# Optimization experiments

Hardware: AMD Instinct MI355X
Metric: run time of the kernel (lower is better)

Reference implementation:

```python
import jax, jax.numpy as jnp
import numpy as np

EMBED_DIM = 1024
NUM_HEADS = 16
HEAD_DIM = EMBED_DIM // NUM_HEADS
SCALE = float(np.sqrt(HEAD_DIM))
B, TQ, TK = 2, 2048, 2048


def setup_inputs() -> dict:
    key = jax.random.key(0)
    ks = jax.random.split(key, 16)
    s = 1.0 / np.sqrt(EMBED_DIM)
    inp = {
        "query": jax.random.normal(ks[0], (B, TQ, EMBED_DIM), jnp.float32),
        "key": jax.random.normal(ks[1], (B, TK, EMBED_DIM), jnp.float32),
        "value": jax.random.normal(ks[2], (B, TK, EMBED_DIM), jnp.float32),
        "key_padding_mask": jnp.zeros((B, TK), dtype=bool),
        "Wq": jax.random.uniform(ks[3], (EMBED_DIM, EMBED_DIM), jnp.float32, -s, s),
        "bq": jax.random.uniform(ks[4], (EMBED_DIM,), jnp.float32, -s, s),
        "Wk": jax.random.uniform(ks[5], (EMBED_DIM, EMBED_DIM), jnp.float32, -s, s),
        "bk": jax.random.uniform(ks[6], (EMBED_DIM,), jnp.float32, -s, s),
        "Wv": jax.random.uniform(ks[7], (EMBED_DIM, EMBED_DIM), jnp.float32, -s, s),
        "bv": jax.random.uniform(ks[8], (EMBED_DIM,), jnp.float32, -s, s),
        "Wo": jax.random.uniform(ks[9], (EMBED_DIM, EMBED_DIM), jnp.float32, -s, s),
        "bo": jax.random.uniform(ks[10], (EMBED_DIM,), jnp.float32, -s, s),
        "clr_bias_q": jax.random.normal(ks[11], (NUM_HEADS, 1, HEAD_DIM), jnp.float32) * 0.02,
        "clr_bias_k": jax.random.normal(ks[12], (NUM_HEADS, 1, HEAD_DIM), jnp.float32) * 0.02,
    }
    return inp


def reference(query, key, value, key_padding_mask, Wq, bq, Wk, bk, Wv, bv, Wo, bo,
              clr_bias_q, clr_bias_k):
    Bsz, Tq, _ = query.shape
    Tk = key.shape[1]

    def split_heads(x, W, b, T):
        # Linear (torch convention: x @ W.T + b) then [B, H, T, Dh]
        y = jnp.einsum('bte,fe->btf', x, W) + b
        return y.reshape(Bsz, T, NUM_HEADS, HEAD_DIM).transpose(0, 2, 1, 3)

    q = split_heads(query, Wq, bq, Tq)   # [B,H,Tq,Dh]
    k = split_heads(key, Wk, bk, Tk)     # [B,H,Tk,Dh]
    v = split_heads(value, Wv, bv, Tk)   # [B,H,Tk,Dh]

    # CLR centering + learned bias (Aitchison similarity)
    q_c = q - jnp.mean(q, axis=-1, keepdims=True) + clr_bias_q[None]
    k_c = k - jnp.mean(k, axis=-1, keepdims=True) + clr_bias_k[None]
    scores = jnp.einsum('bhqd,bhkd->bhqk', q_c, k_c) / SCALE  # [B,H,Tq,Tk]

    mask = key_padding_mask[:, None, None, :]  # [B,1,1,Tk], True = ignore
    scores = jnp.where(mask, -jnp.inf, scores)

    attn = jax.nn.softmax(scores, axis=-1)
    out = jnp.einsum('bhqk,bhkd->bhqd', attn, v)
    out = out.transpose(0, 2, 1, 3).reshape(Bsz, Tq, EMBED_DIM)
    return jnp.einsum('bte,fe->btf', out, Wo) + bo
```

## Files before the change

### kernel.cpp

```cpp
#include <hip/hip_runtime.h>
#include <stdint.h>

static constexpr int EMB   = 1024;
static constexpr int HEADS = 16;
static constexpr int HD    = 64;
static constexpr int BATCH = 2;
static constexpr int SEQ   = 2048;
static constexpr int BT    = BATCH * SEQ;
static constexpr float QSC = 0.18033688011112042f;

typedef short   short8  __attribute__((ext_vector_type(8)));
typedef float   float4v __attribute__((ext_vector_type(4)));

__device__ __forceinline__ ushort f2bf(float f) {
    union { float f; uint32_t i; } v; v.f = f;
    uint32_t x = v.i;
    return (ushort)((x + 0x7FFFu + ((x >> 16) & 1u)) >> 16);
}
__device__ __forceinline__ uint32_t pack2bf(float lo, float hi) {
    union { float f; uint32_t u; } a, b; a.f = lo; b.f = hi;
    uint32_t ra = a.u + 0x7FFFu + ((a.u >> 16) & 1u);
    uint32_t rb = b.u + 0x7FFFu + ((b.u >> 16) & 1u);
    return (rb & 0xFFFF0000u) | (ra >> 16);
}
__device__ __forceinline__ float fast_exp2(float x) {
#if __has_builtin(__builtin_amdgcn_exp2f)
    return __builtin_amdgcn_exp2f(x);
#else
    return exp2f(x);
#endif
}

__device__ __forceinline__ void async_ld16(const void* g, void* l) {
    __builtin_amdgcn_global_load_lds(
        (const __attribute__((address_space(1))) void*)g,
        (__attribute__((address_space(3))) void*)l,
        16, 0, 0);
}

__global__ void cvt_all(const float* __restrict__ q, const float* __restrict__ k,
                        const float* __restrict__ v,
                        const float* __restrict__ wq, const float* __restrict__ wk,
                        const float* __restrict__ wv, const float* __restrict__ wo,
                        ushort* __restrict__ qb, ushort* __restrict__ kb,
                        ushort* __restrict__ vb,
                        ushort* __restrict__ wqb, ushort* __restrict__ wkb,
                        ushort* __restrict__ wvb, ushort* __restrict__ wob)
{
    int bid = blockIdx.x;
    const float* src; ushort* dst; size_t off;
    if (bid < 6144) {
        int seg = bid >> 11;
        src = seg == 0 ? q : (seg == 1 ? k : v);
        dst = seg == 0 ? qb : (seg == 1 ? kb : vb);
        off = (size_t)(bid & 2047) * 2048;
    } else {
        int t = bid - 6144, seg = t >> 9;
        src = seg == 0 ? wq : (seg == 1 ? wk : (seg == 2 ? wv : wo));
        dst = seg == 0 ? wqb : (seg == 1 ? wkb : (seg == 2 ? wvb : wob));
        off = (size_t)(t & 511) * 2048;
    }
    size_t base = off + (size_t)threadIdx.x * 8;
    float4 a0 = *(const float4*)(src + base);
    float4 a1 = *(const float4*)(src + base + 4);
    uint32_t o[4] = { pack2bf(a0.x, a0.y), pack2bf(a0.z, a0.w),
                      pack2bf(a1.x, a1.y), pack2bf(a1.z, a1.w) };
    *(uint4*)(dst + base) = *(uint4*)o;
}

__device__ __forceinline__ void gemm_core_128(
    const ushort* __restrict__ A, const ushort* __restrict__ W,
    int m0, int n0, int K,
    ushort* As, ushort* Ws,
    int wid, int lane, float4v acc[4][4])
{
    const int lrow8 = lane >> 3;
    const int gc    = (lane & 7) ^ lrow8;
    const ushort* Ab = A + (size_t)m0 * K + gc * 8;
    const ushort* Wb = W + (size_t)n0 * K + gc * 8;
    const int wm = (wid >> 1) * 64;
    const int wn = (wid & 1) * 64;

    for (int k0 = 0; k0 < K; k0 += 64) {
        __syncthreads();
#pragma unroll
        for (int it = 0; it < 4; ++it) {
            int rg = it * 4 + wid;
            int row = rg * 8 + lrow8;
            async_ld16(Ab + (size_t)row * K + k0, &As[rg * 512]);
            async_ld16(Wb + (size_t)row * K + k0, &Ws[rg * 512]);
        }
        __syncthreads();
#pragma unroll
        for (int ks = 0; ks < 2; ++ks) {
            const int c = ks * 4 + (lane >> 4);
            short8 af[4], wf[4];
#pragma unroll
            for (int i = 0; i < 4; i++) {
                int row = wm + i * 16 + (lane & 15);
                af[i] = *(const short8*)&As[row * 64 + ((c ^ (row & 7)) * 8)];
            }
#pragma unroll
            for (int j = 0; j < 4; j++) {
                int row = wn + j * 16 + (lane & 15);
                wf[j] = *(const short8*)&Ws[row * 64 + ((c ^ (row & 7)) * 8)];
            }
#pragma unroll
            for (int i = 0; i < 4; i++)
#pragma unroll
                for (int j = 0; j < 4; j++)
                    acc[i][j] = __builtin_amdgcn_mfma_f32_16x16x32_bf16(af[i], wf[j], acc[i][j], 0, 0, 0);
        }
    }
}

__global__ __launch_bounds__(256, 3)
void gemm_qkv(const ushort* __restrict__ qb, const ushort* __restrict__ kb,
              const ushort* __restrict__ vb,
              const ushort* __restrict__ wqb, const ushort* __restrict__ wkb,
              const ushort* __restrict__ wvb,
              const float* __restrict__ bq, const float* __restrict__ bk,
              const float* __restrict__ bv,
              const float* __restrict__ cbq, const float* __restrict__ cbk,
              ushort* __restrict__ qc, ushort* __restrict__ kc,
              ushort* __restrict__ vt)
{
    __shared__ __align__(16) ushort As[128 * 64];
    __shared__ __align__(16) ushort Ws[128 * 64];

    const int z = blockIdx.z;
    const ushort* A    = z == 0 ? qb  : (z == 1 ? kb  : vb);
    const ushort* W    = z == 0 ? wqb : (z == 1 ? wkb : wvb);
    const float*  bias = z == 0 ? bq  : (z == 1 ? bk  : bv);
    const float*  clrb = z == 0 ? cbq : cbk;
    const float   scale = z == 0 ? QSC : 1.0f;

    const int tid  = threadIdx.x;
    const int wid  = tid >> 6;
    const int lane = tid & 63;
    const int m0 = blockIdx.y * 128;
    const int n0 = blockIdx.x * 128;
    const int wm = (wid >> 1) * 64;
    const int wn = (wid & 1) * 64;

    float4v acc[4][4];
#pragma unroll
    for (int i = 0; i < 4; i++)
#pragma unroll
        for (int j = 0; j < 4; j++) acc[i][j] = (float4v)0.0f;

    gemm_core_128(A, W, m0, n0, EMB, As, Ws, wid, lane, acc);

    const int h = (n0 + wn) >> 6;
#pragma unroll
    for (int i = 0; i < 4; i++) {
        float ys[4][4];
#pragma unroll
        for (int j = 0; j < 4; j++) {
            float bj = bias[n0 + wn + j * 16 + (lane & 15)];
#pragma unroll
            for (int r = 0; r < 4; r++) ys[j][r] = acc[i][j][r] + bj;
        }
        const int rowb = m0 + wm + i * 16 + ((lane >> 4) << 2);

        if (z < 2) {
            float rs[4];
#pragma unroll
            for (int r = 0; r < 4; r++)
                rs[r] = ys[0][r] + ys[1][r] + ys[2][r] + ys[3][r];
#pragma unroll
            for (int r = 0; r < 4; r++)
#pragma unroll
                for (int off = 1; off < 16; off <<= 1)
                    rs[r] += __shfl_xor(rs[r], off, 64);
            ushort* Yb = z == 0 ? qc : kc;
#pragma unroll
            for (int j = 0; j < 4; j++) {
                int d = j * 16 + (lane & 15);
                float cb = clrb[h * HD + d];
#pragma unroll
                for (int r = 0; r < 4; r++) {
                    int row = rowb + r;
                    int b = row >> 11, t = row & (SEQ - 1);
                    Yb[((size_t)(b * HEADS + h) * SEQ + t) * HD + d] =
                        f2bf((ys[j][r] - rs[r] * (1.0f / 64.0f) + cb) * scale);
                }
            }
        } else {
#pragma unroll
            for (int j = 0; j < 4; j++) {
                int d = j * 16 + (lane & 15);
#pragma unroll
                for (int r = 0; r < 4; r++) {
                    int row = rowb + r;
                    int b = row >> 11, t = row & (SEQ - 1);
                    vt[((size_t)(b * HEADS + h) * HD + d) * SEQ + t] = f2bf(ys[j][r]);
                }
            }
        }
    }
}

__global__ __launch_bounds__(256, 4)
void gemm_out(const ushort* __restrict__ A, const ushort* __restrict__ W,
              const float* __restrict__ bias, float* __restrict__ Y)
{
    __shared__ __align__(16) ushort As[64 * 64];
    __shared__ __align__(16) ushort Ws[64 * 64];

    const int tid  = threadIdx.x;
    const int wid  = tid >> 6;
    const int lane = tid & 63;
    const int m0 = blockIdx.y * 64;
    const int n0 = blockIdx.x * 64;
    const int wm = (wid >> 1) * 32;
    const int wn = (wid & 1) * 32;

    const int lrow8 = lane >> 3;
    const int gc    = (lane & 7) ^ lrow8;
    const ushort* Ab = A + (size_t)m0 * EMB + gc * 8;
    const ushort* Wb = W + (size_t)n0 * EMB + gc * 8;

    float4v acc[2][2];
#pragma unroll
    for (int i = 0; i < 2; i++)
#pragma unroll
        for (int j = 0; j < 2; j++) acc[i][j] = (float4v)0.0f;

    for (int k0 = 0; k0 < EMB; k0 += 64) {
        __syncthreads();
#pragma unroll
        for (int it = 0; it < 2; ++it) {
            int rg = it * 4 + wid;
            int row = rg * 8 + lrow8;
            async_ld16(Ab + (size_t)row * EMB + k0, &As[rg * 512]);
            async_ld16(Wb + (size_t)row * EMB + k0, &Ws[rg * 512]);
        }
        __syncthreads();
#pragma unroll
        for (int ks = 0; ks < 2; ++ks) {
            const int c = ks * 4 + (lane >> 4);
            short8 af[2], wf[2];
#pragma unroll
            for (int i = 0; i < 2; i++) {
                int row = wm + i * 16 + (lane & 15);
                af[i] = *(const short8*)&As[row * 64 + ((c ^ (row & 7)) * 8)];
            }
#pragma unroll
            for (int j = 0; j < 2; j++) {
                int row = wn + j * 16 + (lane & 15);
                wf[j] = *(const short8*)&Ws[row * 64 + ((c ^ (row & 7)) * 8)];
            }
#pragma unroll
            for (int i = 0; i < 2; i++)
#pragma unroll
                for (int j = 0; j < 2; j++)
                    acc[i][j] = __builtin_amdgcn_mfma_f32_16x16x32_bf16(af[i], wf[j], acc[i][j], 0, 0, 0);
        }
    }

#pragma unroll
    for (int i = 0; i < 2; i++) {
        const int rowb = m0 + wm + i * 16 + ((lane >> 4) << 2);
#pragma unroll
        for (int j = 0; j < 2; j++) {
            int col = n0 + wn + j * 16 + (lane & 15);
            float bj = bias[col];
#pragma unroll
            for (int r = 0; r < 4; r++)
                Y[(size_t)(rowb + r) * EMB + col] = acc[i][j][r] + bj;
        }
    }
}

__global__ __launch_bounds__(512, 4)
void attn_kernel(const ushort* __restrict__ qc,
                 const ushort* __restrict__ kc,
                 const ushort* __restrict__ vt,
                 const unsigned char* __restrict__ mask,
                 ushort* __restrict__ out)
{
    __shared__ __align__(16) ushort Ks[2][64 * 64];
    __shared__ __align__(16) ushort Vs[2][64 * 64];
    __shared__ __align__(16) ushort Ps[8][16 * 88];
    __shared__ __align__(16) float  Msk[SEQ];

    const int tid  = threadIdx.x;
    const int wid  = tid >> 6;
    const int lane = tid & 63;
    const int c    = lane & 15;
    const int hi   = lane >> 4;

    const int bid = blockIdx.x;
    const int qt = bid & 15;
    const int h  = (bid >> 4) & 15;
    const int b  = bid >> 8;

    const ushort* qbase = qc + ((size_t)(b * HEADS + h)) * SEQ * HD;
    const ushort* kbase = kc + ((size_t)(b * HEADS + h)) * SEQ * HD;
    const ushort* vbase = vt + ((size_t)(b * HEADS + h)) * HD * SEQ;

    {
        const int k0 = tid * 4;
        uint32_t mv = *(const uint32_t*)(mask + b * SEQ + k0);
#pragma unroll
        for (int i = 0; i < 4; ++i)
            Msk[k0 + i] = ((mv >> (8 * i)) & 0xffu) ? -1e30f : 0.0f;
    }

    const int qrow = qt * 128 + wid * 16 + c;
    short8 qf[2];
#pragma unroll
    for (int ks = 0; ks < 2; ++ks)
        qf[ks] = *(const short8*)(qbase + (size_t)qrow * HD + ks * 32 + hi * 8);

    float l_lane = 0.f;
    float4v o[4];
#pragma unroll
    for (int j = 0; j < 4; j++) o[j] = (float4v)0.f;

    const int lrow8 = lane >> 3;
    const int gc    = (lane & 7) ^ lrow8;
    ushort* Pw = &Ps[wid][0];

#define STAGE(t, sel)                                                          \
    {                                                                          \
        int row = wid * 8 + lrow8;                                             \
        async_ld16(kbase + (size_t)((t) * 64 + row) * HD + gc * 8,             \
                   &Ks[sel][wid * 512]);                                       \
        async_ld16(vbase + (size_t)row * SEQ + (t) * 64 + gc * 8,              \
                   &Vs[sel][wid * 512]);                                       \
    }

    STAGE(0, 0);
    asm volatile("s_waitcnt vmcnt(0)" ::: "memory");
    __syncthreads();

    int cur = 0;
    for (int kt = 0; kt < SEQ / 64; ++kt) {
        if (kt + 1 < SEQ / 64) STAGE(kt + 1, cur ^ 1);

        const ushort* Kc = &Ks[cur][0];
        const ushort* Vc = &Vs[cur][0];

        float4 mz4[4];
#pragma unroll
        for (int j = 0; j < 4; ++j)
            mz4[j] = *(const float4*)&Msk[kt * 64 + j * 16 + 4 * hi];

        float4v s[4];
        __builtin_amdgcn_s_setprio(1);
#pragma unroll
        for (int j = 0; j < 4; j++) {
            s[j] = (float4v)0.f;
#pragma unroll
            for (int ks = 0; ks < 2; ks++) {
                int row = j * 16 + c;
                int cc  = ks * 4 + hi;
                short8 kf = *(const short8*)&Kc[row * 64 + ((cc ^ (row & 7)) * 8)];
                s[j] = __builtin_amdgcn_mfma_f32_16x16x32_bf16(kf, qf[ks], s[j], 0, 0, 0);
            }
        }
        __builtin_amdgcn_s_setprio(0);

#pragma unroll
        for (int j = 0; j < 4; j++) {
            float p0 = fast_exp2(s[j][0] + mz4[j].x);
            float p1 = fast_exp2(s[j][1] + mz4[j].y);
            float p2 = fast_exp2(s[j][2] + mz4[j].z);
            float p3 = fast_exp2(s[j][3] + mz4[j].w);
            l_lane += (p0 + p1) + (p2 + p3);
            uint2 u = { pack2bf(p0, p1), pack2bf(p2, p3) };
            *(uint2*)&Pw[c * 88 + j * 16 + 4 * hi] = u;
        }
        asm volatile("s_waitcnt lgkmcnt(0)" ::: "memory");

        short8 pf[2];
#pragma unroll
        for (int ks = 0; ks < 2; ks++)
            pf[ks] = *(const short8*)&Pw[c * 88 + ks * 32 + hi * 8];

        __builtin_amdgcn_s_setprio(1);
#pragma unroll
        for (int j = 0; j < 4; j++) {
            int d = j * 16 + c;
#pragma unroll
            for (int ks = 0; ks < 2; ks++) {
                int cc = ks * 4 + hi;
                short8 vf = *(const short8*)&Vc[d * 64 + ((cc ^ (d & 7)) * 8)];
                o[j] = __builtin_amdgcn_mfma_f32_16x16x32_bf16(pf[ks], vf, o[j], 0, 0, 0);
            }
        }
        __builtin_amdgcn_s_setprio(0);

        asm volatile("s_waitcnt vmcnt(0)" ::: "memory");
        __syncthreads();
        cur ^= 1;
    }
#undef STAGE

    l_lane += __shfl_xor(l_lane, 16, 64);
    l_lane += __shfl_xor(l_lane, 32, 64);
    float lr[4];
#pragma unroll
    for (int r = 0; r < 4; r++)
        lr[r] = __shfl(l_lane, 4 * hi + r, 64);

    const int qrow_out = qt * 128 + wid * 16 + (hi << 2);
#pragma unroll
    for (int j = 0; j < 4; j++) {
        int d = j * 16 + c;
#pragma unroll
        for (int r = 0; r < 4; r++) {
            float val = o[j][r] / lr[r];
            out[((size_t)(b * SEQ + qrow_out + r)) * EMB + h * HD + d] = f2bf(val);
        }
    }
}

extern "C" void kernel_launch(void* const* d_in, const int* in_sizes, int n_in,
                              void* d_out, int out_size, void* d_ws, size_t ws_size,
                              hipStream_t stream)
{
    const float* query = (const float*)d_in[0];
    const float* key_  = (const float*)d_in[1];
    const float* value = (const float*)d_in[2];
    const unsigned char* mask = (const unsigned char*)d_in[3];
    const float* Wq  = (const float*)d_in[4];
    const float* bq  = (const float*)d_in[5];
    const float* Wk  = (const float*)d_in[6];
    const float* bk  = (const float*)d_in[7];
    const float* Wv  = (const float*)d_in[8];
    const float* bv  = (const float*)d_in[9];
    const float* Wo  = (const float*)d_in[10];
    const float* bo  = (const float*)d_in[11];
    const float* cbq = (const float*)d_in[12];
    const float* cbk = (const float*)d_in[13];

    ushort* ws = (ushort*)d_ws;
    const size_t n1 = (size_t)BT * EMB;
    const size_t nw = (size_t)EMB * EMB;
    ushort* qb  = ws;
    ushort* kb  = qb  + n1;
    ushort* vb  = kb  + n1;
    ushort* wqb = vb  + n1;
    ushort* wkb = wqb + nw;
    ushort* wvb = wkb + nw;
    ushort* wob = wvb + nw;
    ushort* qc  = wob + nw;
    ushort* kc  = qc  + n1;
    ushort* vt  = kc  + n1;
    ushort* ao  = qb;

    cvt_all<<<8192, 256, 0, stream>>>(query, key_, value, Wq, Wk, Wv, Wo,
                                      qb, kb, vb, wqb, wkb, wvb, wob);

    dim3 gq(EMB / 128, BT / 128, 3);
    gemm_qkv<<<gq, 256, 0, stream>>>(qb, kb, vb, wqb, wkb, wvb,
                                     bq, bk, bv, cbq, cbk, qc, kc, vt);

    attn_kernel<<<BATCH * HEADS * (SEQ / 128), 512, 0, stream>>>(qc, kc, vt, mask, ao);

    dim3 go(EMB / 64, BT / 64);
    gemm_out<<<go, 256, 0, stream>>>(ao, wob, bo, (float*)d_out);
}
```

Baseline: 234.9 us.

## Give each attention wave 32 query rows to reuse K/V LDS fragments

The attention block now uses 4 waves of 256 threads instead of 8, and each wave handles two 16-row query sub-tiles. Each K and V fragment read from LDS is reused across both sub-tiles, halving LDS read traffic per MFMA. K/V staging is split into two loads per thread, and the P scratch is resized to 32 rows per wave. The cost is more registers per wave (double accumulators, scores and Q fragments) and fewer waves per block to hide latency.

```diff
diff --git a/kernel.cpp b/kernel.cpp
--- a/kernel.cpp
+++ b/kernel.cpp
@@ -273,7 +273,7 @@
     }
 }
 
-__global__ __launch_bounds__(512, 4)
+__global__ __launch_bounds__(256, 2)
 void attn_kernel(const ushort* __restrict__ qc,
                  const ushort* __restrict__ kc,
                  const ushort* __restrict__ vt,
@@ -282,7 +282,7 @@
 {
     __shared__ __align__(16) ushort Ks[2][64 * 64];
     __shared__ __align__(16) ushort Vs[2][64 * 64];
-    __shared__ __align__(16) ushort Ps[8][16 * 88];
+    __shared__ __align__(16) ushort Ps[4][32 * 72];
     __shared__ __align__(16) float  Msk[SEQ];
 
     const int tid  = threadIdx.x;
@@ -301,23 +301,31 @@
     const ushort* vbase = vt + ((size_t)(b * HEADS + h)) * HD * SEQ;
 
     {
-        const int k0 = tid * 4;
-        uint32_t mv = *(const uint32_t*)(mask + b * SEQ + k0);
+        const int k0 = tid * 8;
+        uint2 mv = *(const uint2*)(mask + b * SEQ + k0);
 #pragma unroll
         for (int i = 0; i < 4; ++i)
-            Msk[k0 + i] = ((mv >> (8 * i)) & 0xffu) ? -1e30f : 0.0f;
-    }
-
-    const int qrow = qt * 128 + wid * 16 + c;
-    short8 qf[2];
-#pragma unroll
-    for (int ks = 0; ks < 2; ++ks)
-        qf[ks] = *(const short8*)(qbase + (size_t)qrow * HD + ks * 32 + hi * 8);
-
-    float l_lane = 0.f;
-    float4v o[4];
-#pragma unroll
-    for (int j = 0; j < 4; j++) o[j] = (float4v)0.f;
+            Msk[k0 + i] = ((mv.x >> (8 * i)) & 0xffu) ? -1e30f : 0.0f;
+#pragma unroll
+        for (int i = 0; i < 4; ++i)
+            Msk[k0 + 4 + i] = ((mv.y >> (8 * i)) & 0xffu) ? -1e30f : 0.0f;
+    }
+
+    short8 qf[2][2];
+#pragma unroll
+    for (int sub = 0; sub < 2; ++sub) {
+        const int qrow = qt * 128 + wid * 32 + sub * 16 + c;
+#pragma unroll
+        for (int ks = 0; ks < 2; ++ks)
+            qf[sub][ks] = *(const short8*)(qbase + (size_t)qrow * HD + ks * 32 + hi * 8);
+    }
+
+    float l_s[2] = {0.f, 0.f};
+    float4v o[2][4];
+#pragma unroll
+    for (int sub = 0; sub < 2; ++sub)
+#pragma unroll
+        for (int j = 0; j < 4; j++) o[sub][j] = (float4v)0.f;
 
     const int lrow8 = lane >> 3;
     const int gc    = (lane & 7) ^ lrow8;
@@ -325,11 +333,15 @@
 
 #define STAGE(t, sel)                                                          \
     {                                                                          \
-        int row = wid * 8 + lrow8;                                             \
-        async_ld16(kbase + (size_t)((t) * 64 + row) * HD + gc * 8,             \
-                   &Ks[sel][wid * 512]);                                       \
-        async_ld16(vbase + (size_t)row * SEQ + (t) * 64 + gc * 8,              \
-                   &Vs[sel][wid * 512]);                                       \
+        _Pragma("unroll")                                                      \
+        for (int it = 0; it < 2; ++it) {                                       \
+            int rg  = it * 4 + wid;                                            \
+            int row = rg * 8 + lrow8;                                          \
+            async_ld16(kbase + (size_t)((t) * 64 + row) * HD + gc * 8,         \
+                       &Ks[sel][rg * 512]);                                    \
+            async_ld16(vbase + (size_t)row * SEQ + (t) * 64 + gc * 8,          \
+                       &Vs[sel][rg * 512]);                                    \
+        }                                                                      \
     }
 
     STAGE(0, 0);
@@ -348,49 +360,70 @@
         for (int j = 0; j < 4; ++j)
             mz4[j] = *(const float4*)&Msk[kt * 64 + j * 16 + 4 * hi];
 
-        float4v s[4];
-        __builtin_amdgcn_s_setprio(1);
-#pragma unroll
-        for (int j = 0; j < 4; j++) {
-            s[j] = (float4v)0.f;
+        short8 kf[4][2];
+#pragma unroll
+        for (int j = 0; j < 4; j++)
 #pragma unroll
             for (int ks = 0; ks < 2; ks++) {
                 int row = j * 16 + c;
                 int cc  = ks * 4 + hi;
-                short8 kf = *(const short8*)&Kc[row * 64 + ((cc ^ (row & 7)) * 8)];
-                s[j] = __builtin_amdgcn_mfma_f32_16x16x32_bf16(kf, qf[ks], s[j], 0, 0, 0);
-            }
-        }
+                kf[j][ks] = *(const short8*)&Kc[row * 64 + ((cc ^ (row & 7)) * 8)];
+            }
+
+        float4v s[2][4];
+        __builtin_amdgcn_s_setprio(1);
+#pragma unroll
+        for (int sub = 0; sub < 2; ++sub)
+#pragma unroll
+            for (int j = 0; j < 4; j++) {
+                s[sub][j] = (float4v)0.f;
+#pragma unroll
+                for (int ks = 0; ks < 2; ks++)
+                    s[sub][j] = __builtin_amdgcn_mfma_f32_16x16x32_bf16(
+                        kf[j][ks], qf[sub][ks], s[sub][j], 0, 0, 0);
+            }
         __builtin_amdgcn_s_setprio(0);
 
 #pragma unroll
-        for (int j = 0; j < 4; j++) {
-            float p0 = fast_exp2(s[j][0] + mz4[j].x);
-            float p1 = fast_exp2(s[j][1] + mz4[j].y);
-            float p2 = fast_exp2(s[j][2] + mz4[j].z);
-            float p3 = fast_exp2(s[j][3] + mz4[j].w);
-            l_lane += (p0 + p1) + (p2 + p3);
-            uint2 u = { pack2bf(p0, p1), pack2bf(p2, p3) };
-            *(uint2*)&Pw[c * 88 + j * 16 + 4 * hi] = u;
-        }
+        for (int sub = 0; sub < 2; ++sub)
+#pragma unroll
+            for (int j = 0; j < 4; j++) {
+                float p0 = fast_exp2(s[sub][j][0] + mz4[j].x);
+                float p1 = fast_exp2(s[sub][j][1] + mz4[j].y);
+                float p2 = fast_exp2(s[sub][j][2] + mz4[j].z);
+                float p3 = fast_exp2(s[sub][j][3] + mz4[j].w);
+                l_s[sub] += (p0 + p1) + (p2 + p3);
+                uint2 u = { pack2bf(p0, p1), pack2bf(p2, p3) };
+                *(uint2*)&Pw[(sub * 16 + c) * 72 + j * 16 + 4 * hi] = u;
+            }
         asm volatile("s_waitcnt lgkmcnt(0)" ::: "memory");
 
-        short8 pf[2];
-#pragma unroll
-        for (int ks = 0; ks < 2; ks++)
-            pf[ks] = *(const short8*)&Pw[c * 88 + ks * 32 + hi * 8];
+        short8 pf[2][2];
+#pragma unroll
+        for (int sub = 0; sub < 2; ++sub)
+#pragma unroll
+            for (int ks = 0; ks < 2; ks++)
+                pf[sub][ks] = *(const short8*)&Pw[(sub * 16 + c) * 72 + ks * 32 + hi * 8];
+
+        short8 vf[4][2];
+#pragma unroll
+        for (int j = 0; j < 4; j++)
+#pragma unroll
+            for (int ks = 0; ks < 2; ks++) {
+                int d  = j * 16 + c;
+                int cc = ks * 4 + hi;
+                vf[j][ks] = *(const short8*)&Vc[d * 64 + ((cc ^ (d & 7)) * 8)];
+            }
 
         __builtin_amdgcn_s_setprio(1);
 #pragma unroll
-        for (int j = 0; j < 4; j++) {
-            int d = j * 16 + c;
-#pragma unroll
-            for (int ks = 0; ks < 2; ks++) {
-                int cc = ks * 4 + hi;
-                short8 vf = *(const short8*)&Vc[d * 64 + ((cc ^ (d & 7)) * 8)];
-                o[j] = __builtin_amdgcn_mfma_f32_16x16x32_bf16(pf[ks], vf, o[j], 0, 0, 0);
-            }
-        }
+        for (int sub = 0; sub < 2; ++sub)
+#pragma unroll
+            for (int j = 0; j < 4; j++)
+#pragma unroll
+                for (int ks = 0; ks < 2; ks++)
+                    o[sub][j] = __builtin_amdgcn_mfma_f32_16x16x32_bf16(
+                        pf[sub][ks], vf[j][ks], o[sub][j], 0, 0, 0);
         __builtin_amdgcn_s_setprio(0);
 
         asm volatile("s_waitcnt vmcnt(0)" ::: "memory");
@@ -399,21 +432,28 @@
     }
 #undef STAGE
 
-    l_lane += __shfl_xor(l_lane, 16, 64);
-    l_lane += __shfl_xor(l_lane, 32, 64);
-    float lr[4];
-#pragma unroll
-    for (int r = 0; r < 4; r++)
-        lr[r] = __shfl(l_lane, 4 * hi + r, 64);
-
-    const int qrow_out = qt * 128 + wid * 16 + (hi << 2);
-#pragma unroll
-    for (int j = 0; j < 4; j++) {
-        int d = j * 16 + c;
-#pragma unroll
-        for (int r = 0; r < 4; r++) {
-            float val = o[j][r] / lr[r];
-            out[((size_t)(b * SEQ + qrow_out + r)) * EMB + h * HD + d] = f2bf(val);
+#pragma unroll
+    for (int sub = 0; sub < 2; ++sub) {
+        l_s[sub] += __shfl_xor(l_s[sub], 16, 64);
+        l_s[sub] += __shfl_xor(l_s[sub], 32, 64);
+    }
+
+#pragma unroll
+    for (int sub = 0; sub < 2; ++sub) {
+        float lr[4];
+#pragma unroll
+        for (int r = 0; r < 4; r++)
+            lr[r] = __shfl(l_s[sub], 4 * hi + r, 64);
+
+        const int qrow_out = qt * 128 + wid * 32 + sub * 16 + (hi << 2);
+#pragma unroll
+        for (int j = 0; j < 4; j++) {
+            int d = j * 16 + c;
+#pragma unroll
+            for (int r = 0; r < 4; r++) {
+                float val = o[sub][j][r] / lr[r];
+                out[((size_t)(b * SEQ + qrow_out + r)) * EMB + h * HD + d] = f2bf(val);
+            }
         }
     }
 }
@@ -459,7 +499,7 @@
     gemm_qkv<<<gq, 256, 0, stream>>>(qb, kb, vb, wqb, wkb, wvb,
                                      bq, bk, bv, cbq, cbk, qc, kc, vt);
 
-    attn_kernel<<<BATCH * HEADS * (SEQ / 128), 512, 0, stream>>>(qc, kc, vt, mask, ao);
+    attn_kernel<<<BATCH * HEADS * (SEQ / 128), 256, 0, stream>>>(qc, kc, vt, mask, ao);
 
     dim3 go(EMB / 64, BT / 64);
     gemm_out<<<go, 256, 0, stream>>>(ao, wob, bo, (float*)d_out);
```

Result: no change. 236.5 us (+0.7%).

## Swap QK MFMA operand order, prefetch mask from global, shrink P buffer

Applied to the files above, without the earlier changes.

The QK^T MFMA now takes operands in (Q,K) order, so each lane holds scores for one key column across four query rows. P is therefore written to LDS as scalar bf16 stores with a 72-element row pitch, and row sums are kept per query row and reduced with a 16-lane butterfly at the end. The LDS mask table is removed; mask bytes for the next tile are prefetched from global memory into registers. This saves LDS and the mask setup, but turns the vectorized P stores into 16 scalar LDS writes per tile and uses a cheaper round-to-nearest bf16 conversion.

```diff
diff --git a/kernel.cpp b/kernel.cpp
--- a/kernel.cpp
+++ b/kernel.cpp
@@ -16,6 +16,10 @@
     union { float f; uint32_t i; } v; v.f = f;
     uint32_t x = v.i;
     return (ushort)((x + 0x7FFFu + ((x >> 16) & 1u)) >> 16);
+}
+__device__ __forceinline__ ushort f2bf_rn(float f) {
+    union { float f; uint32_t i; } v; v.f = f;
+    return (ushort)((v.i + 0x8000u) >> 16);
 }
 __device__ __forceinline__ uint32_t pack2bf(float lo, float hi) {
     union { float f; uint32_t u; } a, b; a.f = lo; b.f = hi;
@@ -282,8 +286,7 @@
 {
     __shared__ __align__(16) ushort Ks[2][64 * 64];
     __shared__ __align__(16) ushort Vs[2][64 * 64];
-    __shared__ __align__(16) ushort Ps[8][16 * 88];
-    __shared__ __align__(16) float  Msk[SEQ];
+    __shared__ __align__(16) ushort Ps[8][16 * 72];
 
     const int tid  = threadIdx.x;
     const int wid  = tid >> 6;
@@ -299,14 +302,7 @@
     const ushort* qbase = qc + ((size_t)(b * HEADS + h)) * SEQ * HD;
     const ushort* kbase = kc + ((size_t)(b * HEADS + h)) * SEQ * HD;
     const ushort* vbase = vt + ((size_t)(b * HEADS + h)) * HD * SEQ;
-
-    {
-        const int k0 = tid * 4;
-        uint32_t mv = *(const uint32_t*)(mask + b * SEQ + k0);
-#pragma unroll
-        for (int i = 0; i < 4; ++i)
-            Msk[k0 + i] = ((mv >> (8 * i)) & 0xffu) ? -1e30f : 0.0f;
-    }
+    const unsigned char* mbase = mask + b * SEQ;
 
     const int qrow = qt * 128 + wid * 16 + c;
     short8 qf[2];
@@ -314,7 +310,7 @@
     for (int ks = 0; ks < 2; ++ks)
         qf[ks] = *(const short8*)(qbase + (size_t)qrow * HD + ks * 32 + hi * 8);
 
-    float l_lane = 0.f;
+    float l_r[4] = {0.f, 0.f, 0.f, 0.f};
     float4v o[4];
 #pragma unroll
     for (int j = 0; j < 4; j++) o[j] = (float4v)0.f;
@@ -332,6 +328,10 @@
                    &Vs[sel][wid * 512]);                                       \
     }
 
+    uint32_t mcur[4], mnext[4];
+#pragma unroll
+    for (int j = 0; j < 4; ++j)
+        mcur[j] = mbase[j * 16 + c];
     STAGE(0, 0);
     asm volatile("s_waitcnt vmcnt(0)" ::: "memory");
     __syncthreads();
@@ -339,14 +339,18 @@
     int cur = 0;
     for (int kt = 0; kt < SEQ / 64; ++kt) {
         if (kt + 1 < SEQ / 64) STAGE(kt + 1, cur ^ 1);
+        const int tn = (kt + 1 < SEQ / 64) ? kt + 1 : kt;
+#pragma unroll
+        for (int j = 0; j < 4; ++j)
+            mnext[j] = mbase[tn * 64 + j * 16 + c];
 
         const ushort* Kc = &Ks[cur][0];
         const ushort* Vc = &Vs[cur][0];
 
-        float4 mz4[4];
+        float mzv[4];
 #pragma unroll
         for (int j = 0; j < 4; ++j)
-            mz4[j] = *(const float4*)&Msk[kt * 64 + j * 16 + 4 * hi];
+            mzv[j] = mcur[j] ? -1e30f : 0.0f;
 
         float4v s[4];
         __builtin_amdgcn_s_setprio(1);
@@ -358,27 +362,27 @@
                 int row = j * 16 + c;
                 int cc  = ks * 4 + hi;
                 short8 kf = *(const short8*)&Kc[row * 64 + ((cc ^ (row & 7)) * 8)];
-                s[j] = __builtin_amdgcn_mfma_f32_16x16x32_bf16(kf, qf[ks], s[j], 0, 0, 0);
+                s[j] = __builtin_amdgcn_mfma_f32_16x16x32_bf16(qf[ks], kf, s[j], 0, 0, 0);
             }
         }
         __builtin_amdgcn_s_setprio(0);
 
 #pragma unroll
         for (int j = 0; j < 4; j++) {
-            float p0 = fast_exp2(s[j][0] + mz4[j].x);
-            float p1 = fast_exp2(s[j][1] + mz4[j].y);
-            float p2 = fast_exp2(s[j][2] + mz4[j].z);
-            float p3 = fast_exp2(s[j][3] + mz4[j].w);
-            l_lane += (p0 + p1) + (p2 + p3);
-            uint2 u = { pack2bf(p0, p1), pack2bf(p2, p3) };
-            *(uint2*)&Pw[c * 88 + j * 16 + 4 * hi] = u;
+            int prow = (hi << 2) * 72 + j * 16 + c;
+#pragma unroll
+            for (int r = 0; r < 4; r++) {
+                float p = fast_exp2(s[j][r] + mzv[j]);
+                l_r[r] += p;
+                Pw[prow + r * 72] = f2bf_rn(p);
+            }
         }
         asm volatile("s_waitcnt lgkmcnt(0)" ::: "memory");
 
         short8 pf[2];
 #pragma unroll
         for (int ks = 0; ks < 2; ks++)
-            pf[ks] = *(const short8*)&Pw[c * 88 + ks * 32 + hi * 8];
+            pf[ks] = *(const short8*)&Pw[c * 72 + ks * 32 + hi * 8];
 
         __builtin_amdgcn_s_setprio(1);
 #pragma unroll
@@ -396,15 +400,17 @@
         asm volatile("s_waitcnt vmcnt(0)" ::: "memory");
         __syncthreads();
         cur ^= 1;
+#pragma unroll
+        for (int j = 0; j < 4; ++j)
+            mcur[j] = mnext[j];
     }
 #undef STAGE
 
-    l_lane += __shfl_xor(l_lane, 16, 64);
-    l_lane += __shfl_xor(l_lane, 32, 64);
-    float lr[4];
 #pragma unroll
     for (int r = 0; r < 4; r++)
-        lr[r] = __shfl(l_lane, 4 * hi + r, 64);
+#pragma unroll
+        for (int off = 1; off < 16; off <<= 1)
+            l_r[r] += __shfl_xor(l_r[r], off, 64);
 
     const int qrow_out = qt * 128 + wid * 16 + (hi << 2);
 #pragma unroll
@@ -412,7 +418,7 @@
         int d = j * 16 + c;
 #pragma unroll
         for (int r = 0; r < 4; r++) {
-            float val = o[j][r] / lr[r];
+            float val = o[j][r] / l_r[r];
             out[((size_t)(b * SEQ + qrow_out + r)) * EMB + h * HD + d] = f2bf(val);
         }
     }
```

Measured after the change: 230.4 us. About the same (-1.9%).
